# Kernel tuning notes

Hardware: AMD Instinct MI355X
Metric: run time of the kernel (lower is better)

The kernel has to match this reference:

```python
import jax, jax.numpy as jnp
import numpy as np

B, L, D, S = 8, 512, 64, 8


def setup_inputs() -> dict:
    key = jax.random.key(0)
    ks = jax.random.split(key, 8)
    return {
        "lstm1": jax.random.normal(ks[0], (B, L, D), dtype=jnp.float32),
        "lstm2": jax.random.normal(ks[1], (B, L, D), dtype=jnp.float32),
        "W": jax.random.normal(ks[2], (S, D, D), dtype=jnp.float32) * 0.1,
        "V": jax.random.normal(ks[3], (S, 2 * D), dtype=jnp.float32) * 0.1,
        "b": jax.random.normal(ks[4], (S,), dtype=jnp.float32) * 0.1,
        "W_g": jax.random.normal(ks[5], (S, 2 * D), dtype=jnp.float32) * 0.1,
        "b_g": jax.random.normal(ks[6], (S,), dtype=jnp.float32) * 0.1,
        "u": jax.random.normal(ks[7], (1, S), dtype=jnp.float32) * 0.1,
    }


def reference(lstm1, lstm2, W, V, b, W_g, b_g, u):
    # lstm1/lstm2: (B, L, D). Pairwise slot (i, j) pairs lstm1[:, i] with lstm2[:, j].
    d = lstm1.shape[-1]
    # Bilinear tensor-network score: x1_i W_s x2_j -> (B, L, L, S)
    result_w = jnp.einsum('bid,sde,bje->bijs', lstm1, W, lstm2)
    # concat(x1_i, x2_j) @ V^T decomposed to avoid materializing (B,L,L,2D)
    v1 = jnp.einsum('bid,sd->bis', lstm1, V[:, :d])[:, :, None, :]   # (B,L,1,S)
    v2 = jnp.einsum('bjd,sd->bjs', lstm2, V[:, d:])[:, None, :, :]   # (B,1,L,S)
    result_v = v1 + v2                                               # (B,L,L,S)
    g1 = jnp.einsum('bid,sd->bis', lstm1, W_g[:, :d])[:, :, None, :]
    g2 = jnp.einsum('bjd,sd->bjs', lstm2, W_g[:, d:])[:, None, :, :]
    gate = jax.nn.sigmoid(g1 + g2 + b_g)                             # (B,L,L,S)
    result_final = gate * result_w + (1.0 - gate) * jax.nn.sigmoid(result_v) + b
    # Reduce slices with u (shape (1,S)) -> (B,L,L), then add singleton channel dim.
    out = jnp.einsum('bijs,ks->bijk', result_final, u)[..., 0]
    return out[:, None, :, :]  # (B, 1, L, L)
```

## Files before the change

### kernel.cpp

```cpp
#include <hip/hip_runtime.h>
#include <math.h>

typedef float f32x4 __attribute__((ext_vector_type(4)));
typedef short bf16x8 __attribute__((ext_vector_type(8)));

namespace {
constexpr int kB = 8, kL = 512, kD = 64, kS = 8;
constexpr size_t SCL_OFF = 0;
constexpr size_t U_OFF   = 524288;
}

__device__ __forceinline__ unsigned short f2bf(float f) {
    unsigned u = __float_as_uint(f);
    u += 0x7FFFu + ((u >> 16) & 1u);
    return (unsigned short)(u >> 16);
}
__device__ __forceinline__ unsigned pk2(float lo, float hi) {
    return (unsigned)f2bf(lo) | ((unsigned)f2bf(hi) << 16);
}
__device__ __forceinline__ bf16x8 ldcvt8(const float* __restrict__ p) {
    const float4 a = *(const float4*)p;
    const float4 b = *(const float4*)(p + 4);
    union { bf16x8 v; uint4 q; } cv;
    cv.q.x = pk2(a.x, a.y); cv.q.y = pk2(a.z, a.w);
    cv.q.z = pk2(b.x, b.y); cv.q.w = pk2(b.z, b.w);
    return cv.v;
}

__global__ __launch_bounds__(256) void grn_a(
    const float* __restrict__ lstm1, const float* __restrict__ lstm2,
    const float* __restrict__ W, const float* __restrict__ V,
    const float* __restrict__ Wg, const float* __restrict__ bg,
    unsigned char* __restrict__ ws)
{
    __shared__ __align__(16) unsigned short tls[4][16][72];
    float* scl = (float*)(ws + SCL_OFF);
    unsigned short* Ut = (unsigned short*)(ws + U_OFF);
    const int tid = threadIdx.x;
    if (blockIdx.x < 64) {
        const int rb = blockIdx.x;
        const int b = rb >> 3, r0 = (rb & 7) * 64;
        const int kind = tid & 3, row = r0 + (tid >> 2);
        const float* x = (kind < 2 ? lstm1 : lstm2) + ((size_t)b * kL + row) * kD;
        float xr[64];
        #pragma unroll
        for (int q = 0; q < 16; q++)
            *(float4*)&xr[q * 4] = *(const float4*)(x + q * 4);
        const float* vb = ((kind & 1) ? Wg : V) + ((kind & 2) ? kD : 0);
        #pragma unroll
        for (int s = 0; s < kS; s++) {
            const float* vec = vb + s * 2 * kD;
            float a = 0.f;
            #pragma unroll
            for (int q = 0; q < 16; q++) {
                const float4 vv = *(const float4*)(vec + q * 4);
                a = fmaf(vv.x, xr[q * 4 + 0], a);
                a = fmaf(vv.y, xr[q * 4 + 1], a);
                a = fmaf(vv.z, xr[q * 4 + 2], a);
                a = fmaf(vv.w, xr[q * 4 + 3], a);
            }
            const float badd = (kind == 1) ? bg[s] : 0.f;
            scl[(((size_t)kind * 8 + b) * 8 + s) * 512 + row] = __expf(-(a + badd));
        }
        return;
    }
    const int t = blockIdx.x - 64;
    const int b = t >> 6, rem = t & 63, s = rem >> 3, j64 = rem & 7;
    const int lane = tid & 63, w = tid >> 6;
    const int fr = lane & 15, fh = lane >> 4;
    const int j0 = j64 * 64 + w * 16;
    const float* bp = lstm2 + (((size_t)b * kL + j0 + fr) * kD + fh * 8);
    const bf16x8 B0 = ldcvt8(bp);
    const bf16x8 B1 = ldcvt8(bp + 32);
    unsigned short (*__restrict__ tw)[72] = tls[w];
    #pragma unroll
    for (int dt = 0; dt < 4; dt++) {
        const float* ap = W + ((size_t)s * 4096 + (dt * 16 + fr) * kD + fh * 8);
        const bf16x8 A0 = ldcvt8(ap);
        const bf16x8 A1 = ldcvt8(ap + 32);
        f32x4 z = {0.f, 0.f, 0.f, 0.f};
        f32x4 d = __builtin_amdgcn_mfma_f32_16x16x32_bf16(A0, B0, z, 0, 0, 0);
        d = __builtin_amdgcn_mfma_f32_16x16x32_bf16(A1, B1, d, 0, 0, 0);
        #pragma unroll
        for (int r = 0; r < 4; r++)
            tw[fr][dt * 16 + fh * 4 + r] = f2bf(d[r]);
    }
    const int rr = lane >> 2, cc = (lane & 3) * 16;
    const uint4 q0 = *(const uint4*)&tw[rr][cc];
    const uint4 q1 = *(const uint4*)&tw[rr][cc + 8];
    unsigned short* up = Ut + (((size_t)(b * 8 + s)) * kL + j0 + rr) * kD + cc;
    *(uint4*)up = q0;
    *(uint4*)(up + 8) = q1;
}

__global__ __launch_bounds__(256) void grn_b(
    const float* __restrict__ lstm1, const float* __restrict__ bS,
    const float* __restrict__ u, const unsigned char* __restrict__ ws,
    float* __restrict__ out)
{
    const float* scl = (const float*)(ws + SCL_OFF);
    const unsigned short* Ut = (const unsigned short*)(ws + U_OFF);
    const int swz = (blockIdx.x & 7) * 128 + (blockIdx.x >> 3);
    const int g = swz * 4 + (threadIdx.x >> 6);
    const int b = g >> 9, rem = g & 511, i32 = rem >> 5, jt = rem & 31;
    const int lane = threadIdx.x & 63, fr = lane & 15, fh = lane >> 4;
    const int i0 = i32 * 32, j0 = jt * 16;
    bf16x8 A[2][2];
    #pragma unroll
    for (int ii = 0; ii < 2; ii++) {
        const float* ap = lstm1 + (((size_t)b * kL + i0 + ii * 16 + fr) * kD + fh * 8);
        A[ii][0] = ldcvt8(ap);
        A[ii][1] = ldcvt8(ap + 32);
    }
    float bias_c = 0.f;
    #pragma unroll
    for (int s = 0; s < kS; s++) bias_c = fmaf(u[s], bS[s], bias_c);
    f32x4 oacc[2];
    oacc[0] = f32x4{bias_c, bias_c, bias_c, bias_c};
    oacc[1] = oacc[0];
    #pragma unroll
    for (int s = 0; s < kS; s++) {
        const unsigned short* bp = Ut + (((size_t)(b * 8 + s)) * kL + j0 + fr) * kD + fh * 8;
        const bf16x8 B0 = *(const bf16x8*)bp;
        const bf16x8 B1 = *(const bf16x8*)(bp + 32);
        const float E2v = scl[(((size_t)2 * 8 + b) * 8 + s) * 512 + j0 + fr];
        const float E2g = scl[(((size_t)3 * 8 + b) * 8 + s) * 512 + j0 + fr];
        const float us = u[s];
        #pragma unroll
        for (int ii = 0; ii < 2; ii++) {
            f32x4 z = {0.f, 0.f, 0.f, 0.f};
            f32x4 acc = __builtin_amdgcn_mfma_f32_16x16x32_bf16(A[ii][0], B0, z, 0, 0, 0);
            acc = __builtin_amdgcn_mfma_f32_16x16x32_bf16(A[ii][1], B1, acc, 0, 0, 0);
            const int ib = i0 + ii * 16 + fh * 4;
            const float4 E1vq = *(const float4*)(scl + (((size_t)0 * 8 + b) * 8 + s) * 512 + ib);
            const float4 E1gq = *(const float4*)(scl + (((size_t)1 * 8 + b) * 8 + s) * 512 + ib);
            const float E1va[4] = {E1vq.x, E1vq.y, E1vq.z, E1vq.w};
            const float E1ga[4] = {E1gq.x, E1gq.y, E1gq.z, E1gq.w};
            #pragma unroll
            for (int r = 0; r < 4; r++) {
                const float dg = fmaf(E1ga[r], E2g, 1.f);
                const float dv = fmaf(E1va[r], E2v, 1.f);
                const float rp = __builtin_amdgcn_rcpf(dg * dv);
                const float gate = dv * rp;
                const float sv   = dg * rp;
                const float res = fmaf(gate, acc[r] - sv, sv);
                oacc[ii][r] = fmaf(us, res, oacc[ii][r]);
            }
        }
    }
    #pragma unroll
    for (int ii = 0; ii < 2; ii++) {
        float* op = out + (((size_t)b * kL + i0 + ii * 16 + fh * 4) * kL + j0 + fr);
        #pragma unroll
        for (int r = 0; r < 4; r++)
            op[(size_t)r * kL] = oacc[ii][r];
    }
}

extern "C" void kernel_launch(void* const* d_in, const int* in_sizes, int n_in,
                              void* d_out, int out_size, void* d_ws, size_t ws_size,
                              hipStream_t stream) {
    const float* lstm1 = (const float*)d_in[0];
    const float* lstm2 = (const float*)d_in[1];
    const float* W     = (const float*)d_in[2];
    const float* V     = (const float*)d_in[3];
    const float* bS    = (const float*)d_in[4];
    const float* Wg    = (const float*)d_in[5];
    const float* bg    = (const float*)d_in[6];
    const float* u     = (const float*)d_in[7];
    unsigned char* ws = (unsigned char*)d_ws;
    grn_a<<<576, 256, 0, stream>>>(lstm1, lstm2, W, V, Wg, bg, ws);
    grn_b<<<1024, 256, 0, stream>>>(lstm1, bS, u, ws, (float*)d_out);
}
```

Before: 106.3 us.

## Enlarge per-wave output tile to 32x32 and stage stores through LDS

Each wave in the second kernel now computes a 32x32 output tile instead of 32x16. The lstm1 A fragments and the E1 scale loads are reused across two column sub-tiles, and the grid is halved. Results are written to a padded per-wave LDS buffer and read back so that global stores become row-contiguous float4 writes instead of scattered 64-byte segments. In exchange it uses more registers and LDS. The float4 reads from rows padded to a 33-float stride are not 16-byte aligned, which depends on the hardware handling unaligned LDS access.

```diff
diff --git a/kernel.cpp b/kernel.cpp
--- a/kernel.cpp
+++ b/kernel.cpp
@@ -98,13 +98,15 @@
     const float* __restrict__ u, const unsigned char* __restrict__ ws,
     float* __restrict__ out)
 {
+    __shared__ float ob[4][32][33];
     const float* scl = (const float*)(ws + SCL_OFF);
     const unsigned short* Ut = (const unsigned short*)(ws + U_OFF);
-    const int swz = (blockIdx.x & 7) * 128 + (blockIdx.x >> 3);
-    const int g = swz * 4 + (threadIdx.x >> 6);
-    const int b = g >> 9, rem = g & 511, i32 = rem >> 5, jt = rem & 31;
+    const int swz = (blockIdx.x & 7) * 64 + (blockIdx.x >> 3);
+    const int w = threadIdx.x >> 6;
+    const int g = swz * 4 + w;
+    const int b = g >> 8, rem = g & 255, i32t = rem >> 4, j32t = rem & 15;
     const int lane = threadIdx.x & 63, fr = lane & 15, fh = lane >> 4;
-    const int i0 = i32 * 32, j0 = jt * 16;
+    const int i0 = i32t * 32, j0 = j32t * 32;
     bf16x8 A[2][2];
     #pragma unroll
     for (int ii = 0; ii < 2; ii++) {
@@ -115,45 +117,64 @@
     float bias_c = 0.f;
     #pragma unroll
     for (int s = 0; s < kS; s++) bias_c = fmaf(u[s], bS[s], bias_c);
-    f32x4 oacc[2];
-    oacc[0] = f32x4{bias_c, bias_c, bias_c, bias_c};
-    oacc[1] = oacc[0];
+    f32x4 oacc[2][2];
+    oacc[0][0] = f32x4{bias_c, bias_c, bias_c, bias_c};
+    oacc[0][1] = oacc[0][0]; oacc[1][0] = oacc[0][0]; oacc[1][1] = oacc[0][0];
     #pragma unroll
     for (int s = 0; s < kS; s++) {
         const unsigned short* bp = Ut + (((size_t)(b * 8 + s)) * kL + j0 + fr) * kD + fh * 8;
-        const bf16x8 B0 = *(const bf16x8*)bp;
-        const bf16x8 B1 = *(const bf16x8*)(bp + 32);
-        const float E2v = scl[(((size_t)2 * 8 + b) * 8 + s) * 512 + j0 + fr];
-        const float E2g = scl[(((size_t)3 * 8 + b) * 8 + s) * 512 + j0 + fr];
+        bf16x8 Bf[2][2];
+        #pragma unroll
+        for (int jj = 0; jj < 2; jj++) {
+            Bf[jj][0] = *(const bf16x8*)(bp + jj * 16 * kD);
+            Bf[jj][1] = *(const bf16x8*)(bp + jj * 16 * kD + 32);
+        }
         const float us = u[s];
+        float E2v[2], E2g[2];
+        #pragma unroll
+        for (int jj = 0; jj < 2; jj++) {
+            E2v[jj] = scl[(((size_t)2 * 8 + b) * 8 + s) * 512 + j0 + jj * 16 + fr];
+            E2g[jj] = scl[(((size_t)3 * 8 + b) * 8 + s) * 512 + j0 + jj * 16 + fr];
+        }
         #pragma unroll
         for (int ii = 0; ii < 2; ii++) {
-            f32x4 z = {0.f, 0.f, 0.f, 0.f};
-            f32x4 acc = __builtin_amdgcn_mfma_f32_16x16x32_bf16(A[ii][0], B0, z, 0, 0, 0);
-            acc = __builtin_amdgcn_mfma_f32_16x16x32_bf16(A[ii][1], B1, acc, 0, 0, 0);
             const int ib = i0 + ii * 16 + fh * 4;
             const float4 E1vq = *(const float4*)(scl + (((size_t)0 * 8 + b) * 8 + s) * 512 + ib);
             const float4 E1gq = *(const float4*)(scl + (((size_t)1 * 8 + b) * 8 + s) * 512 + ib);
             const float E1va[4] = {E1vq.x, E1vq.y, E1vq.z, E1vq.w};
             const float E1ga[4] = {E1gq.x, E1gq.y, E1gq.z, E1gq.w};
             #pragma unroll
-            for (int r = 0; r < 4; r++) {
-                const float dg = fmaf(E1ga[r], E2g, 1.f);
-                const float dv = fmaf(E1va[r], E2v, 1.f);
-                const float rp = __builtin_amdgcn_rcpf(dg * dv);
-                const float gate = dv * rp;
-                const float sv   = dg * rp;
-                const float res = fmaf(gate, acc[r] - sv, sv);
-                oacc[ii][r] = fmaf(us, res, oacc[ii][r]);
+            for (int jj = 0; jj < 2; jj++) {
+                f32x4 z = {0.f, 0.f, 0.f, 0.f};
+                f32x4 acc = __builtin_amdgcn_mfma_f32_16x16x32_bf16(A[ii][0], Bf[jj][0], z, 0, 0, 0);
+                acc = __builtin_amdgcn_mfma_f32_16x16x32_bf16(A[ii][1], Bf[jj][1], acc, 0, 0, 0);
+                #pragma unroll
+                for (int r = 0; r < 4; r++) {
+                    const float dg = fmaf(E1ga[r], E2g[jj], 1.f);
+                    const float dv = fmaf(E1va[r], E2v[jj], 1.f);
+                    const float rp = __builtin_amdgcn_rcpf(dg * dv);
+                    const float gate = dv * rp;
+                    const float sv   = dg * rp;
+                    const float res = fmaf(gate, acc[r] - sv, sv);
+                    oacc[ii][jj][r] = fmaf(us, res, oacc[ii][jj][r]);
+                }
             }
         }
     }
+    float (*__restrict__ ot)[33] = ob[w];
     #pragma unroll
-    for (int ii = 0; ii < 2; ii++) {
-        float* op = out + (((size_t)b * kL + i0 + ii * 16 + fh * 4) * kL + j0 + fr);
+    for (int ii = 0; ii < 2; ii++)
         #pragma unroll
-        for (int r = 0; r < 4; r++)
-            op[(size_t)r * kL] = oacc[ii][r];
+        for (int jj = 0; jj < 2; jj++)
+            #pragma unroll
+            for (int r = 0; r < 4; r++)
+                ot[ii * 16 + fh * 4 + r][jj * 16 + fr] = oacc[ii][jj][r];
+    #pragma unroll
+    for (int p = 0; p < 4; p++) {
+        const int f = p * 64 + lane;
+        const int row = f >> 3, c4 = (f & 7) * 4;
+        const float4 v = *(const float4*)&ot[row][c4];
+        *(float4*)(out + (((size_t)b * kL + i0 + row) * kL + j0 + c4)) = v;
     }
 }
 
@@ -170,5 +191,5 @@
     const float* u     = (const float*)d_in[7];
     unsigned char* ws = (unsigned char*)d_ws;
     grn_a<<<576, 256, 0, stream>>>(lstm1, lstm2, W, V, Wg, bg, ws);
-    grn_b<<<1024, 256, 0, stream>>>(lstm1, bS, u, ws, (float*)d_out);
+    grn_b<<<512, 256, 0, stream>>>(lstm1, bS, u, ws, (float*)d_out);
 }
```

Result: faster. 102.0 us (-4.1%).
